# Kernel optimization log

Hardware: AMD Instinct MI355X
Metric: run time of the kernel (lower is better)

The kernel has to match this reference:

```python
import jax, jax.numpy as jnp
import numpy as np

SCALE = 8.0  # sqrt(hid=64), passed as init arg `scale`


def setup_inputs() -> dict:
    key = jax.random.key(0)
    kq, kk, kv, km = jax.random.split(key, 4)
    B, S, H = 32, 2048, 64  # B = bs*n_head
    q = jax.random.normal(kq, (B, S, H), dtype=jnp.float32)
    k = jax.random.normal(kk, (B, S, H), dtype=jnp.float32)
    v = jax.random.normal(kv, (B, S, H), dtype=jnp.float32)
    mask = jax.random.bernoulli(km, 0.1, (B, S, S))  # True = masked out
    return {"q": q, "k": k, "v": v, "mask": mask, "cca": 0}


def reference(q, k, v, mask, cca):
    # scores: [B, Sq, Sk]
    attn = jnp.einsum('bqh,bkh->bqk', q, k) / SCALE
    if mask is not None:
        attn = jnp.where(mask, jnp.finfo(q.dtype).min, attn)
    if cca:
        # CCA branch: softmax over the query/sequence axis (dim=1)
        attn = jax.nn.softmax(attn, axis=1)
        ctx = jnp.einsum('bq,bkh->bqh', attn.squeeze(-1)[..., None].squeeze(-1), v) if attn.ndim == 2 else jnp.einsum('bqk,bkh->bqh', attn, v)
    else:
        attn = jax.nn.softmax(attn, axis=2)
        ctx = jnp.einsum('bqk,bkh->bqh', attn, v)  # [B, Sq, H]
    return (ctx, attn)
```

## Files before the change

### kernel.cpp

```cpp
#include <hip/hip_runtime.h>
#include <hip/hip_bf16.h>

typedef __bf16    bf16x8_t __attribute__((ext_vector_type(8)));
typedef float     f32x4_t  __attribute__((ext_vector_type(4)));
typedef short     s16x4_t  __attribute__((ext_vector_type(4)));
typedef short     s16x8_t  __attribute__((ext_vector_type(8)));
typedef unsigned  u32x4_t  __attribute__((ext_vector_type(4)));

#define S_LEN 2048
#define HDIM  64
#define BQ    32
#define NTHREADS 512
#define PSTR_B 4112
#define BMSTR 264

__device__ __forceinline__ short f2bf(float f) {
    return __builtin_bit_cast(short, (__bf16)f);
}
__device__ __forceinline__ float bf2f(short s) {
    return __builtin_bit_cast(float, ((unsigned)(unsigned short)s) << 16);
}
__device__ __forceinline__ short* pelem(short* P, int row, int e) {
    return (short*)((char*)P + (unsigned)row * PSTR_B + (unsigned)e * 2u);
}
__device__ __forceinline__ const short* pelemc(const short* P, int row, int e) {
    return pelem(const_cast<short*>(P), row, e);
}
__device__ __forceinline__ unsigned nzmask16(u32x4_t w) {
    unsigned n = 0;
    #pragma unroll
    for (int i = 0; i < 4; ++i) {
        const unsigned x = w[i];
        const unsigned t = (x & 0x7F7F7F7Fu) + 0x7F7F7F7Fu;
        const unsigned z = ((t | x) & 0x80808080u) >> 7;
        n |= ((z * 0x10204081u) >> 28) << (4 * i);
    }
    return n;
}
__device__ __forceinline__ unsigned nzmask4w(u32x4_t w) {
    return (w[0] ? 1u : 0u) | (w[1] ? 2u : 0u) | (w[2] ? 4u : 0u) | (w[3] ? 8u : 0u);
}

#define PK8(lo, hi, out8) { s16x8_t _t; \
    _t[0]=f2bf((lo)[0]); _t[1]=f2bf((lo)[1]); _t[2]=f2bf((lo)[2]); _t[3]=f2bf((lo)[3]); \
    _t[4]=f2bf((hi)[0]); _t[5]=f2bf((hi)[1]); _t[6]=f2bf((hi)[2]); _t[7]=f2bf((hi)[3]); \
    (out8) = __builtin_bit_cast(bf16x8_t, _t); }
#define PKV(src, dst) { s16x8_t _t; \
    _t[0]=f2bf((src)[0]); _t[1]=f2bf((src)[1]); _t[2]=f2bf((src)[2]); _t[3]=f2bf((src)[3]); \
    _t[4]=f2bf((src)[4]); _t[5]=f2bf((src)[5]); _t[6]=f2bf((src)[6]); _t[7]=f2bf((src)[7]); \
    (dst) = __builtin_bit_cast(bf16x8_t, _t); }

__global__ void detect_mask(const unsigned char* __restrict__ M, int* __restrict__ flags) {
    __shared__ int cnt[4];
    if (threadIdx.x < 4) cnt[threadIdx.x] = 0;
    __syncthreads();
    int local[4] = {0, 0, 0, 0};
    for (int i = threadIdx.x; i < 16384; i += 256)
        if (M[i]) local[i & 3]++;
    #pragma unroll
    for (int c = 0; c < 4; ++c)
        if (local[c]) atomicAdd(&cnt[c], local[c]);
    __syncthreads();
    if (threadIdx.x == 0) {
        int stride;
        if (cnt[1] == 0 && cnt[2] == 0 && cnt[3] == 0)      stride = 4;
        else if (cnt[0] == 0 && cnt[1] == 0)                stride = 4;
        else                                                stride = 1;
        flags[0] = stride;
    }
}

__global__ __launch_bounds__(NTHREADS, 2)
void sdpa_one(const float* __restrict__ Q, const float* __restrict__ K,
              const float* __restrict__ V, const unsigned char* __restrict__ M,
              const int* __restrict__ MF, float* __restrict__ OUT)
{
    __shared__ short Plds[BQ * (PSTR_B / 2)];
    __shared__ unsigned char Bm[BQ * BMSTR];
    __shared__ float Pvp[4][BQ][17];
    __shared__ float rowsum[BQ];
    __shared__ float rinv_s[BQ];

    const int tid  = threadIdx.x;
    const int w    = tid >> 6;
    const int lane = tid & 63;
    const int col  = lane & 15;
    const int kg   = lane >> 4;
    const int mstride = MF[0];

    const int id   = blockIdx.x;
    const int slot = id >> 3;
    const int b    = ((slot >> 6) << 3) | (id & 7);
    const int q0   = (slot & 63) * BQ;

    float* attn_out = OUT + (size_t)32 * S_LEN * HDIM;

    if (tid < BQ) rowsum[tid] = 0.f;

    {
        const int row  = tid >> 4;
        const int segE = (tid & 15) * 128;
        unsigned long long bits[2] = {0ull, 0ull};
        if (mstride == 1) {
            const unsigned char* mp = M + (size_t)b * S_LEN * S_LEN
                                        + (size_t)(q0 + row) * S_LEN + segE;
            #pragma unroll 1
            for (int j = 0; j < 8; ++j)
                bits[j >> 2] |= (unsigned long long)nzmask16(*(const u32x4_t*)(mp + j * 16))
                                << (16 * (j & 3));
        } else {
            const unsigned* mp = (const unsigned*)M + (size_t)b * S_LEN * S_LEN
                                   + (size_t)(q0 + row) * S_LEN + segE;
            #pragma unroll 1
            for (int j = 0; j < 32; ++j)
                bits[j >> 4] |= (unsigned long long)nzmask4w(*(const u32x4_t*)(mp + j * 4))
                                << (4 * (j & 15));
        }
        unsigned long long* bp = (unsigned long long*)&Bm[row * BMSTR + (tid & 15) * 16];
        bp[0] = bits[0]; bp[1] = bits[1];
    }

    bf16x8_t af[2][2];
    #pragma unroll
    for (int m = 0; m < 2; ++m)
        #pragma unroll
        for (int kk = 0; kk < 2; ++kk) {
            const float* qp = Q + ((size_t)b * S_LEN + q0 + m * 16 + col) * HDIM + kk * 32 + kg * 8;
            const f32x4_t qa = *(const f32x4_t*)qp;
            const f32x4_t qb = *(const f32x4_t*)(qp + 4);
            PK8(qa, qb, af[m][kk]);
        }
    __syncthreads();

    float rs0 = 0.f, rs1 = 0.f;
    {
        const float* Kb = K + (size_t)b * S_LEN * HDIM;
        f32x4_t A0,B0,C0,D0, A1,B1,C1,D1;
#define LDK(f, AX,BX,CX,DX) { \
    const float* kp = Kb + (size_t)(w * 256 + (f) * 16 + col) * HDIM + kg * 8; \
    AX = *(const f32x4_t*)kp;        BX = *(const f32x4_t*)(kp + 4); \
    CX = *(const f32x4_t*)(kp + 32); DX = *(const f32x4_t*)(kp + 36); }
#define STEP(f, AX,BX,CX,DX, PF, fp) { \
    bf16x8_t kb0, kb1; PK8(AX, BX, kb0); PK8(CX, DX, kb1); \
    if (PF) LDK(fp, AX,BX,CX,DX); \
    f32x4_t acc0 = {0.f,0.f,0.f,0.f}, acc1 = {0.f,0.f,0.f,0.f}; \
    acc0 = __builtin_amdgcn_mfma_f32_16x16x32_bf16(kb0, af[0][0], acc0, 0,0,0); \
    acc0 = __builtin_amdgcn_mfma_f32_16x16x32_bf16(kb1, af[0][1], acc0, 0,0,0); \
    acc1 = __builtin_amdgcn_mfma_f32_16x16x32_bf16(kb0, af[1][0], acc1, 0,0,0); \
    acc1 = __builtin_amdgcn_mfma_f32_16x16x32_bf16(kb1, af[1][1], acc1, 0,0,0); \
    const int c0 = w * 256 + (f) * 16 + kg * 4; \
    const int sh = c0 & 7; \
    { const unsigned bb = Bm[col * BMSTR + (c0 >> 3)]; \
      float p0 = ((bb >> (sh    )) & 1u) ? 0.f : __expf(acc0[0] * 0.125f); \
      float p1 = ((bb >> (sh + 1)) & 1u) ? 0.f : __expf(acc0[1] * 0.125f); \
      float p2 = ((bb >> (sh + 2)) & 1u) ? 0.f : __expf(acc0[2] * 0.125f); \
      float p3 = ((bb >> (sh + 3)) & 1u) ? 0.f : __expf(acc0[3] * 0.125f); \
      rs0 += (p0 + p1) + (p2 + p3); \
      s16x4_t pk; pk[0]=f2bf(p0); pk[1]=f2bf(p1); pk[2]=f2bf(p2); pk[3]=f2bf(p3); \
      *(s16x4_t*)pelem(Plds, col, c0) = pk; } \
    { const unsigned bb = Bm[(16 + col) * BMSTR + (c0 >> 3)]; \
      float p0 = ((bb >> (sh    )) & 1u) ? 0.f : __expf(acc1[0] * 0.125f); \
      float p1 = ((bb >> (sh + 1)) & 1u) ? 0.f : __expf(acc1[1] * 0.125f); \
      float p2 = ((bb >> (sh + 2)) & 1u) ? 0.f : __expf(acc1[2] * 0.125f); \
      float p3 = ((bb >> (sh + 3)) & 1u) ? 0.f : __expf(acc1[3] * 0.125f); \
      rs1 += (p0 + p1) + (p2 + p3); \
      s16x4_t pk; pk[0]=f2bf(p0); pk[1]=f2bf(p1); pk[2]=f2bf(p2); pk[3]=f2bf(p3); \
      *(s16x4_t*)pelem(Plds, 16 + col, c0) = pk; } }
        LDK(0, A0,B0,C0,D0);
        LDK(1, A1,B1,C1,D1);
        #pragma unroll 1
        for (int ff = 0; ff < 16; ff += 2) {
            STEP(ff,     A0,B0,C0,D0, (ff + 2 < 16), ff + 2);
            STEP(ff + 1, A1,B1,C1,D1, (ff + 3 < 16), ff + 3);
        }
#undef LDK
#undef STEP
    }
    {
        float s0 = rs0, s1 = rs1;
        s0 += __shfl_xor(s0, 16); s0 += __shfl_xor(s0, 32);
        s1 += __shfl_xor(s1, 16); s1 += __shfl_xor(s1, 32);
        if (lane < 16) {
            atomicAdd(&rowsum[col], s0);
            atomicAdd(&rowsum[16 + col], s1);
        }
    }
    __syncthreads();
    if (tid < BQ) rinv_s[tid] = 1.0f / rowsum[tid];
    __syncthreads();

    const int hb    = (w & 3) * 16;
    const int kbase = (w >> 2) * 1024;
    const float* Vb = V + (size_t)b * S_LEN * HDIM;

    f32x4_t cacc0 = {0.f,0.f,0.f,0.f}, cacc1 = {0.f,0.f,0.f,0.f};
    {
        float vr0[8], vr1[8];
#define LOADV(kc, dst) { \
    const float* vp = Vb + (size_t)(kbase + (kc) * 32 + kg * 8) * HDIM + hb + col; \
    dst[0] = vp[0];        dst[1] = vp[HDIM];     dst[2] = vp[2*HDIM]; dst[3] = vp[3*HDIM]; \
    dst[4] = vp[4*HDIM];   dst[5] = vp[5*HDIM];   dst[6] = vp[6*HDIM]; dst[7] = vp[7*HDIM]; }
#define PVSTEP(kc, vsrc) { \
    bf16x8_t vbf; PKV(vsrc, vbf); \
    const int ke = kbase + (kc) * 32 + kg * 8; \
    const bf16x8_t pa0 = *(const bf16x8_t*)pelemc(Plds, col,      ke); \
    const bf16x8_t pa1 = *(const bf16x8_t*)pelemc(Plds, 16 + col, ke); \
    cacc0 = __builtin_amdgcn_mfma_f32_16x16x32_bf16(pa0, vbf, cacc0, 0,0,0); \
    cacc1 = __builtin_amdgcn_mfma_f32_16x16x32_bf16(pa1, vbf, cacc1, 0,0,0); }
        LOADV(0, vr0); LOADV(1, vr1);
        #pragma unroll 1
        for (int kc = 0; kc < 30; kc += 2) {
            PVSTEP(kc,     vr0); LOADV(kc + 2, vr0);
            PVSTEP(kc + 1, vr1); LOADV(kc + 3, vr1);
        }
        PVSTEP(30, vr0);
        PVSTEP(31, vr1);
#undef LOADV
#undef PVSTEP
    }

    {
        const int srow = w * 4 + kg;
        const float my_rinv = rinv_s[srow];
        float* abp = attn_out + ((size_t)b * S_LEN + q0 + srow) * S_LEN + col * 4;
        #pragma unroll 1
        for (int sec = 0; sec < 32; ++sec) {
            const s16x4_t pv = *(const s16x4_t*)pelemc(Plds, srow, sec * 64 + col * 4);
            f32x4_t o;
            o[0] = bf2f(pv[0]) * my_rinv; o[1] = bf2f(pv[1]) * my_rinv;
            o[2] = bf2f(pv[2]) * my_rinv; o[3] = bf2f(pv[3]) * my_rinv;
            *(f32x4_t*)(abp + sec * 64) = o;
        }
    }

    if (w >= 4) {
        #pragma unroll
        for (int r = 0; r < 4; ++r) {
            Pvp[w - 4][kg * 4 + r][col]      = cacc0[r];
            Pvp[w - 4][16 + kg * 4 + r][col] = cacc1[r];
        }
    }
    __syncthreads();
    if (w < 4) {
        #pragma unroll
        for (int r = 0; r < 4; ++r) {
            const int row0 = kg * 4 + r;
            const int row1 = 16 + kg * 4 + r;
            OUT[((size_t)b * S_LEN + q0 + row0) * HDIM + hb + col]
                = (cacc0[r] + Pvp[w][row0][col]) * rinv_s[row0];
            OUT[((size_t)b * S_LEN + q0 + row1) * HDIM + hb + col]
                = (cacc1[r] + Pvp[w][row1][col]) * rinv_s[row1];
        }
    }
}

extern "C" void kernel_launch(void* const* d_in, const int* in_sizes, int n_in,
                              void* d_out, int out_size, void* d_ws, size_t ws_size,
                              hipStream_t stream)
{
    const float* q = (const float*)d_in[0];
    const float* k = (const float*)d_in[1];
    const float* v = (const float*)d_in[2];
    const unsigned char* mask = (const unsigned char*)d_in[3];
    int* mflags = (int*)d_ws;
    float* out = (float*)d_out;
    detect_mask<<<dim3(1), dim3(256), 0, stream>>>(mask, mflags);
    sdpa_one<<<dim3(2048), dim3(NTHREADS), 0, stream>>>(q, k, v, mask, mflags, out);
}
```

Before: 465.7 us.

## Double block to 1024 threads and reduce PV partials via LDS atomics

Doubles the threads per block to 16 waves and halves each wave's share of key columns, mask bits, PV k-range and attention-row writeout. The PV partial sums from the four k-ranges are now combined with LDS atomicAdd into a full 32x64 buffer, replacing the two-stage Pvp reduction. Loops are fully unrolled. Launch bounds drop to one block per CU, so the number of resident waves per CU stays the same while per-wave serial work shrinks. In exchange it adds atomic contention and an extra zeroing pass over the buffer.

```diff
diff --git a/kernel.cpp b/kernel.cpp
--- a/kernel.cpp
+++ b/kernel.cpp
@@ -10,7 +10,7 @@
 #define S_LEN 2048
 #define HDIM  64
 #define BQ    32
-#define NTHREADS 512
+#define NTHREADS 1024
 #define PSTR_B 4112
 #define BMSTR 264
 
@@ -70,14 +70,14 @@
     }
 }
 
-__global__ __launch_bounds__(NTHREADS, 2)
+__global__ __launch_bounds__(NTHREADS, 1)
 void sdpa_one(const float* __restrict__ Q, const float* __restrict__ K,
               const float* __restrict__ V, const unsigned char* __restrict__ M,
               const int* __restrict__ MF, float* __restrict__ OUT)
 {
     __shared__ short Plds[BQ * (PSTR_B / 2)];
     __shared__ unsigned char Bm[BQ * BMSTR];
-    __shared__ float Pvp[4][BQ][17];
+    __shared__ float Pvx[BQ][HDIM];
     __shared__ float rowsum[BQ];
     __shared__ float rinv_s[BQ];
 
@@ -96,28 +96,32 @@
     float* attn_out = OUT + (size_t)32 * S_LEN * HDIM;
 
     if (tid < BQ) rowsum[tid] = 0.f;
-
-    {
-        const int row  = tid >> 4;
-        const int segE = (tid & 15) * 128;
-        unsigned long long bits[2] = {0ull, 0ull};
+    {
+        float* pz = &Pvx[0][0];
+        pz[tid] = 0.f;
+        pz[tid + 1024] = 0.f;
+    }
+
+    {
+        const int row  = tid >> 5;
+        const int segE = (tid & 31) * 64;
+        unsigned long long bits = 0ull;
         if (mstride == 1) {
             const unsigned char* mp = M + (size_t)b * S_LEN * S_LEN
                                         + (size_t)(q0 + row) * S_LEN + segE;
-            #pragma unroll 1
-            for (int j = 0; j < 8; ++j)
-                bits[j >> 2] |= (unsigned long long)nzmask16(*(const u32x4_t*)(mp + j * 16))
-                                << (16 * (j & 3));
+            #pragma unroll
+            for (int j = 0; j < 4; ++j)
+                bits |= (unsigned long long)nzmask16(*(const u32x4_t*)(mp + j * 16))
+                        << (16 * j);
         } else {
             const unsigned* mp = (const unsigned*)M + (size_t)b * S_LEN * S_LEN
                                    + (size_t)(q0 + row) * S_LEN + segE;
-            #pragma unroll 1
-            for (int j = 0; j < 32; ++j)
-                bits[j >> 4] |= (unsigned long long)nzmask4w(*(const u32x4_t*)(mp + j * 4))
-                                << (4 * (j & 15));
-        }
-        unsigned long long* bp = (unsigned long long*)&Bm[row * BMSTR + (tid & 15) * 16];
-        bp[0] = bits[0]; bp[1] = bits[1];
+            #pragma unroll
+            for (int j = 0; j < 16; ++j)
+                bits |= (unsigned long long)nzmask4w(*(const u32x4_t*)(mp + j * 4))
+                        << (4 * j);
+        }
+        *(unsigned long long*)&Bm[row * BMSTR + (segE >> 3)] = bits;
     }
 
     bf16x8_t af[2][2];
@@ -137,7 +141,7 @@
         const float* Kb = K + (size_t)b * S_LEN * HDIM;
         f32x4_t A0,B0,C0,D0, A1,B1,C1,D1;
 #define LDK(f, AX,BX,CX,DX) { \
-    const float* kp = Kb + (size_t)(w * 256 + (f) * 16 + col) * HDIM + kg * 8; \
+    const float* kp = Kb + (size_t)(w * 128 + (f) * 16 + col) * HDIM + kg * 8; \
     AX = *(const f32x4_t*)kp;        BX = *(const f32x4_t*)(kp + 4); \
     CX = *(const f32x4_t*)(kp + 32); DX = *(const f32x4_t*)(kp + 36); }
 #define STEP(f, AX,BX,CX,DX, PF, fp) { \
@@ -148,7 +152,7 @@
     acc0 = __builtin_amdgcn_mfma_f32_16x16x32_bf16(kb1, af[0][1], acc0, 0,0,0); \
     acc1 = __builtin_amdgcn_mfma_f32_16x16x32_bf16(kb0, af[1][0], acc1, 0,0,0); \
     acc1 = __builtin_amdgcn_mfma_f32_16x16x32_bf16(kb1, af[1][1], acc1, 0,0,0); \
-    const int c0 = w * 256 + (f) * 16 + kg * 4; \
+    const int c0 = w * 128 + (f) * 16 + kg * 4; \
     const int sh = c0 & 7; \
     { const unsigned bb = Bm[col * BMSTR + (c0 >> 3)]; \
       float p0 = ((bb >> (sh    )) & 1u) ? 0.f : __expf(acc0[0] * 0.125f); \
@@ -168,10 +172,10 @@
       *(s16x4_t*)pelem(Plds, 16 + col, c0) = pk; } }
         LDK(0, A0,B0,C0,D0);
         LDK(1, A1,B1,C1,D1);
-        #pragma unroll 1
-        for (int ff = 0; ff < 16; ff += 2) {
-            STEP(ff,     A0,B0,C0,D0, (ff + 2 < 16), ff + 2);
-            STEP(ff + 1, A1,B1,C1,D1, (ff + 3 < 16), ff + 3);
+        #pragma unroll
+        for (int ff = 0; ff < 8; ff += 2) {
+            STEP(ff,     A0,B0,C0,D0, (ff + 2 < 8), ff + 2);
+            STEP(ff + 1, A1,B1,C1,D1, (ff + 3 < 8), ff + 3);
         }
 #undef LDK
 #undef STEP
@@ -190,7 +194,7 @@
     __syncthreads();
 
     const int hb    = (w & 3) * 16;
-    const int kbase = (w >> 2) * 1024;
+    const int kbase = (w >> 2) * 512;
     const float* Vb = V + (size_t)b * S_LEN * HDIM;
 
     f32x4_t cacc0 = {0.f,0.f,0.f,0.f}, cacc1 = {0.f,0.f,0.f,0.f};
@@ -208,49 +212,46 @@
     cacc0 = __builtin_amdgcn_mfma_f32_16x16x32_bf16(pa0, vbf, cacc0, 0,0,0); \
     cacc1 = __builtin_amdgcn_mfma_f32_16x16x32_bf16(pa1, vbf, cacc1, 0,0,0); }
         LOADV(0, vr0); LOADV(1, vr1);
-        #pragma unroll 1
-        for (int kc = 0; kc < 30; kc += 2) {
+        #pragma unroll
+        for (int kc = 0; kc < 14; kc += 2) {
             PVSTEP(kc,     vr0); LOADV(kc + 2, vr0);
             PVSTEP(kc + 1, vr1); LOADV(kc + 3, vr1);
         }
-        PVSTEP(30, vr0);
-        PVSTEP(31, vr1);
+        PVSTEP(14, vr0);
+        PVSTEP(15, vr1);
 #undef LOADV
 #undef PVSTEP
     }
-
-    {
-        const int srow = w * 4 + kg;
+    #pragma unroll
+    for (int r = 0; r < 4; ++r) {
+        atomicAdd(&Pvx[kg * 4 + r][hb + col],      cacc0[r]);
+        atomicAdd(&Pvx[16 + kg * 4 + r][hb + col], cacc1[r]);
+    }
+
+    {
+        const int srow = w * 2 + (lane >> 5);
+        const int lc   = lane & 31;
         const float my_rinv = rinv_s[srow];
-        float* abp = attn_out + ((size_t)b * S_LEN + q0 + srow) * S_LEN + col * 4;
-        #pragma unroll 1
-        for (int sec = 0; sec < 32; ++sec) {
-            const s16x4_t pv = *(const s16x4_t*)pelemc(Plds, srow, sec * 64 + col * 4);
+        float* abp = attn_out + ((size_t)b * S_LEN + q0 + srow) * S_LEN + lc * 4;
+        #pragma unroll 4
+        for (int sec = 0; sec < 16; ++sec) {
+            const s16x4_t pv = *(const s16x4_t*)pelemc(Plds, srow, sec * 128 + lc * 4);
             f32x4_t o;
             o[0] = bf2f(pv[0]) * my_rinv; o[1] = bf2f(pv[1]) * my_rinv;
             o[2] = bf2f(pv[2]) * my_rinv; o[3] = bf2f(pv[3]) * my_rinv;
-            *(f32x4_t*)(abp + sec * 64) = o;
-        }
-    }
-
-    if (w >= 4) {
-        #pragma unroll
-        for (int r = 0; r < 4; ++r) {
-            Pvp[w - 4][kg * 4 + r][col]      = cacc0[r];
-            Pvp[w - 4][16 + kg * 4 + r][col] = cacc1[r];
-        }
-    }
-    __syncthreads();
-    if (w < 4) {
-        #pragma unroll
-        for (int r = 0; r < 4; ++r) {
-            const int row0 = kg * 4 + r;
-            const int row1 = 16 + kg * 4 + r;
-            OUT[((size_t)b * S_LEN + q0 + row0) * HDIM + hb + col]
-                = (cacc0[r] + Pvp[w][row0][col]) * rinv_s[row0];
-            OUT[((size_t)b * S_LEN + q0 + row1) * HDIM + hb + col]
-                = (cacc1[r] + Pvp[w][row1][col]) * rinv_s[row1];
-        }
+            *(f32x4_t*)(abp + sec * 128) = o;
+        }
+    }
+
+    __syncthreads();
+    {
+        const int row = tid >> 5;
+        const int c0  = (tid & 31) * 2;
+        const float ri = rinv_s[row];
+        float2 o;
+        o.x = Pvx[row][c0]     * ri;
+        o.y = Pvx[row][c0 + 1] * ri;
+        *(float2*)(OUT + ((size_t)b * S_LEN + q0 + row) * HDIM + c0) = o;
     }
 }
 
```

New measurement: 451.7 us. -3.0%, faster.
